# Kernel tuning notes

Measured on AMD Instinct MI355X. Metric: run time of the kernel, lower is better.

The kernel has to match this reference:

```python
import jax, jax.numpy as jnp
import numpy as np

ANCHORS = np.array([10,13,16,30,33,23,30,61,62,45,59,119,116,90,156,198,373,326], np.float32).reshape(-1, 2)
ANCHOR_MASK = ((6, 7, 8), (3, 4, 5), (0, 1, 2))
INPUT_SHAPE = (416.0, 416.0)
NUM_BOX = 3
NUM_CLASSES = 80
LOC_RATIO, CLS_RATIO, CONF_RATIO = 0.05, 0.5, 1.0
BALANCE = (0.4, 1.0, 4.0)
EPS = 1e-7


def _bce(p, t):
    p = jnp.clip(p, EPS, 1.0 - EPS)
    return -t * jnp.log(p) - (1.0 - t) * jnp.log(1.0 - p)


def _build_targets(i, targets_xywh, targets_cls, H, W):
    # Vectorized version of get_target: per-box anchor argmax-IoU matching
    # followed by scatter writes into the [B, 3, H, W, 5+C] target tensor.
    B, T, _ = targets_xywh.shape
    sy, sx = INPUT_SHAPE[0] / H, INPUT_SHAPE[1] / W
    sa = jnp.asarray(ANCHORS / np.array([sx, sy], np.float32))  # [9,2] scaled anchors
    bx = targets_xywh[..., 0] * W
    by = targets_xywh[..., 1] * H
    bw = targets_xywh[..., 2] * W
    bh = targets_xywh[..., 3] * H
    # IoU of zero-centered gt boxes vs zero-centered anchors reduces to min(w)*min(h)
    inter = jnp.minimum(bw[..., None], sa[:, 0]) * jnp.minimum(bh[..., None], sa[:, 1])
    union = (bw * bh)[..., None] + sa[:, 0] * sa[:, 1] - inter
    aid = jnp.argmax(inter / union, axis=-1)  # [B,T] best anchor of 9
    mrow = jnp.asarray(ANCHOR_MASK[i])  # i is a static Python int
    hit = aid[..., None] == mrow  # [B,T,3]
    valid = hit.any(-1)
    pos = jnp.argmax(hit, axis=-1)  # anchor_pos_id within this layer's mask
    gx = jnp.floor(bx).astype(jnp.int32)
    gy = jnp.floor(by).astype(jnp.int32)
    b_idx = jnp.broadcast_to(jnp.arange(B)[:, None], (B, T))
    b_sc = jnp.where(valid, b_idx, B)  # out-of-range batch index -> dropped scatter
    tw = jnp.log(bw / sa[aid, 0])
    th = jnp.log(bh / sa[aid, 1])
    y_true = jnp.zeros((B, NUM_BOX, H, W, 5 + NUM_CLASSES), jnp.float32)
    y_true = y_true.at[b_sc, pos, gy, gx, 0].set(bx - gx, mode='drop')
    y_true = y_true.at[b_sc, pos, gy, gx, 1].set(by - gy, mode='drop')
    y_true = y_true.at[b_sc, pos, gy, gx, 2].set(tw, mode='drop')
    y_true = y_true.at[b_sc, pos, gy, gx, 3].set(th, mode='drop')
    y_true = y_true.at[b_sc, pos, gy, gx, 5 + targets_cls].set(1.0, mode='drop')
    y_true = y_true.at[b_sc, pos, gy, gx, 4].set(1.0, mode='drop')
    loss_scale = jnp.zeros((B, NUM_BOX, H, W), jnp.float32)
    loss_scale = loss_scale.at[b_sc, pos, gy, gx].set(bw * bh / (H * W), mode='drop')
    return y_true, loss_scale


def setup_inputs() -> dict:
    key = jax.random.key(0)
    k1, k2, k3, k4 = jax.random.split(key, 4)
    B, T, H, W = 32, 50, 52, 52
    pred = jax.random.normal(k1, (B, NUM_BOX * (5 + NUM_CLASSES), H, W), jnp.float32) * 0.5
    xy = jax.random.uniform(k2, (B, T, 2), jnp.float32, 0.02, 0.98)
    wh = jax.random.uniform(k3, (B, T, 2), jnp.float32, 0.02, 0.5)
    targets_xywh = jnp.concatenate([xy, wh], axis=-1)
    targets_cls = jax.random.randint(k4, (B, T), 0, NUM_CLASSES, jnp.int32)
    return {"i": 2, "pred": pred, "targets_xywh": targets_xywh, "targets_cls": targets_cls}


def reference(i, pred, targets_xywh, targets_cls):
    B = pred.shape[0]
    H, W = pred.shape[-2:]
    y_true, loss_scale = _build_targets(i, targets_xywh, targets_cls, H, W)
    y_true = jax.lax.stop_gradient(y_true)  # torch builds these with requires_grad=False
    loss_scale = jax.lax.stop_gradient(loss_scale)
    # [B, 3*(5+C), H, W] -> [B, 3, H, W, 5+C]
    p = pred.reshape(B, NUM_BOX, 5 + NUM_CLASSES, H, W).transpose(0, 1, 3, 4, 2)
    x = jax.nn.sigmoid(p[..., 0])
    y = jax.nn.sigmoid(p[..., 1])
    w = p[..., 2]
    h = p[..., 3]
    conf = jax.nn.sigmoid(p[..., 4])
    cls_prob = jax.nn.sigmoid(p[..., 5:])
    scale = 2.0 - loss_scale
    m = (y_true[..., 4] == 1).astype(jnp.float32)
    pos_num = m.sum()
    den = jnp.maximum(pos_num, 1.0)
    lx = (_bce(x, y_true[..., 0]) * scale * m).sum() / den
    ly = (_bce(y, y_true[..., 1]) * scale * m).sum() / den
    lw = (jnp.square(w - y_true[..., 2]) * scale * m).sum() / den
    lh = (jnp.square(h - y_true[..., 3]) * scale * m).sum() / den
    loc_loss = (lx + ly + lh + lw) * 0.1
    cls_loss = (_bce(cls_prob, y_true[..., 5:]) * m[..., None]).sum() / (den * NUM_CLASSES)
    conf_loss = _bce(conf, y_true[..., 4]).mean() * BALANCE[i]
    has = pos_num > 0
    total = jnp.where(has, loc_loss * LOC_RATIO + cls_loss * CLS_RATIO, 0.0) + conf_loss * CONF_RATIO
    return jnp.stack([total, conf_loss, jnp.where(has, loc_loss, 0.0), jnp.where(has, cls_loss, 0.0)])
```

## Files before the change

### kernel.cpp

```cpp
#include <hip/hip_runtime.h>
#include <math.h>

#define BB 32
#define TT 50
#define HH 52
#define WW 52
#define NB 3
#define NC 80
#define CE 85
#define SP (HH*WW)
#define NCELL (BB*NB*SP)
#define NT (BB*TT)
#define EPSF 1e-7f

#define NBLK 507
#define POSBLK 100

__device__ __forceinline__ float sigc(float z) {
    float p = 1.0f / (1.0f + expf(-z));
    return fminf(fmaxf(p, EPSF), 1.0f - EPSF);
}

__device__ __forceinline__ float softplus(float z) {
    return fmaxf(z, 0.0f) + log1pf(expf(-fabsf(z)));
}

__device__ __forceinline__ unsigned getbit(unsigned m0, unsigned m1, unsigned m2, int c) {
    return (c < 32) ? ((m0 >> c) & 1u)
         : (c < 64) ? ((m1 >> (c - 32)) & 1u)
                    : ((m2 >> (c - 64)) & 1u);
}

__device__ __forceinline__ int match_target(const float* __restrict__ xywh,
                                            const int* __restrict__ cls,
                                            int i, int w,
                                            float* obx, float* oby,
                                            float* obw, float* obh, int* oaid) {
    const float A[18] = {10,13,16,30,33,23,30,61,62,45,59,119,116,90,156,198,373,326};
    float bx = xywh[w*4+0] * WW, by = xywh[w*4+1] * HH;
    float bw = xywh[w*4+2] * WW, bh = xywh[w*4+3] * HH;
    int aid = 0;
    float bi = -1.0f, bu = 1.0f;
    #pragma unroll
    for (int k = 0; k < 9; ++k) {
        float aw = A[2*k] * 0.125f, ah = A[2*k+1] * 0.125f;
        float inter = fminf(bw, aw) * fminf(bh, ah);
        float uni = bw * bh + aw * ah - inter;
        if (inter * bu > bi * uni) { bi = inter; bu = uni; aid = k; }
    }
    *obx = bx; *oby = by; *obw = bw; *obh = bh; *oaid = aid;
    int gx = (int)floorf(bx), gy = (int)floorf(by);
    if ((aid / 3) == (2 - i) && gx >= 0 && gx < WW && gy >= 0 && gy < HH) {
        int b = w / TT;
        int cell = ((b * NB + (aid % 3)) * HH + gy) * WW + gx;
        return (cell << 7) | cls[w];
    }
    return -1;
}

__global__ void __launch_bounds__(256)
k_main(const float* __restrict__ pred,
       const float* __restrict__ xywh,
       const int* __restrict__ cls,
       const int* __restrict__ pi,
       float* __restrict__ confpart,
       float* __restrict__ pospart) {
    __shared__ int epack[NT];
    __shared__ float sred[4];
    __shared__ float pred_red[4][8];
    int tid = threadIdx.x;
    int bid = blockIdx.x;
    int lane = tid & 63;
    int wid = tid >> 6;

    int base = (bid * 256 + tid) * 2;
    int ba = base / SP, sp = base % SP;
    float2 z2 = *(const float2*)(pred + ((size_t)ba * CE + 4) * SP + sp);
    float vconf = softplus(z2.x) + softplus(z2.y);

    if (bid < POSBLK) {
        int i = *pi;
        for (int w = tid; w < NT; w += 256) {
            float bx, by, bw, bh; int aid;
            epack[w] = match_target(xywh, cls, i, w, &bx, &by, &bw, &bh, &aid);
        }
        __syncthreads();

        float zprim[4], zsec[4];
        bool tval[4];
        #pragma unroll
        for (int t = 0; t < 4; ++t) {
            int wv = bid * 16 + wid * 4 + t;
            int ep = epack[wv];
            tval[t] = (ep >= 0);
            zprim[t] = 0.0f; zsec[t] = 0.0f;
            if (ep >= 0) {
                int cell = ep >> 7;
                int cba = cell / SP, csp = cell % SP;
                const float* pc = pred + (size_t)cba * CE * SP + csp;
                zprim[t] = pc[lane * SP];
                if (lane < CE - 64) zsec[t] = pc[(64 + lane) * SP];
            }
        }

        float acc[7] = {0.f, 0.f, 0.f, 0.f, 0.f, 0.f, 0.f};
        #pragma unroll
        for (int t = 0; t < 4; ++t) {
            if (!tval[t]) continue;
            int wv = bid * 16 + wid * 4 + t;
            int cell = epack[wv] >> 7;
            unsigned m0 = 0, m1 = 0, m2 = 0;
            int mx = -1;
            #pragma unroll
            for (int k = 0; k < NT / 64; ++k) {
                int e = lane + 64 * k;
                int ee = epack[e];
                if (ee >= 0 && (ee >> 7) == cell) {
                    int c = ee & 127;
                    if (c < 32) m0 |= 1u << c;
                    else if (c < 64) m1 |= 1u << (c - 32);
                    else m2 |= 1u << (c - 64);
                    mx = max(mx, e);
                }
            }
            #pragma unroll
            for (int off = 32; off; off >>= 1) {
                m0 |= __shfl_xor(m0, off);
                m1 |= __shfl_xor(m1, off);
                m2 |= __shfl_xor(m2, off);
                mx = max(mx, __shfl_xor(mx, off));
            }
            if (mx != wv) continue;

            const float A[18] = {10,13,16,30,33,23,30,61,62,45,59,119,116,90,156,198,373,326};
            float bx, by, bw, bh; int aid;
            (void)match_target(xywh, cls, i, wv, &bx, &by, &bw, &bh, &aid);
            float aw = A[2*aid] * 0.125f, ah = A[2*aid+1] * 0.125f;
            float gx = floorf(bx), gy = floorf(by);
            float tx = bx - gx, ty = by - gy;
            float tw = logf(bw / aw), th = logf(bh / ah);
            float scale = 2.0f - bw * bh / (float)(HH * WW);

            float z = zprim[t];
            float p = sigc(z);
            float prim;
            if (lane == 0)      prim = (-tx * logf(p) - (1.0f - tx) * logf(1.0f - p)) * scale;
            else if (lane == 1) prim = (-ty * logf(p) - (1.0f - ty) * logf(1.0f - p)) * scale;
            else if (lane == 2) { float d = z - tw; prim = d * d * scale; }
            else if (lane == 3) { float d = z - th; prim = d * d * scale; }
            else if (lane == 4) prim = -logf(p) + logf(1.0f - p);
            else {
                int c = lane - 5;
                prim = getbit(m0, m1, m2, c) ? -logf(p) : -logf(1.0f - p);
            }
            float sec = 0.0f;
            if (lane < CE - 64) {
                float pc2 = sigc(zsec[t]);
                sec = getbit(m0, m1, m2, 59 + lane) ? -logf(pc2) : -logf(1.0f - pc2);
            }
            float clsv = (lane >= 5 ? prim : 0.0f) + sec;
            #pragma unroll
            for (int off = 32; off; off >>= 1) clsv += __shfl_xor(clsv, off);
            acc[0] += __shfl(prim, 0);
            acc[1] += __shfl(prim, 1);
            acc[2] += __shfl(prim, 2);
            acc[3] += __shfl(prim, 3);
            acc[4] += __shfl(prim, 4);
            acc[5] += clsv;
            acc[6] += 1.0f;
        }
        if (lane == 0) {
            #pragma unroll
            for (int k = 0; k < 7; ++k) pred_red[wid][k] = acc[k];
        }
        __syncthreads();
        if (tid == 0) {
            float r[7];
            #pragma unroll
            for (int k = 0; k < 7; ++k)
                r[k] = pred_red[0][k] + pred_red[1][k] + pred_red[2][k] + pred_red[3][k];
            float4 a = make_float4(r[0], r[1], r[2], r[3]);
            float4 b = make_float4(r[4], r[5], r[6], 0.0f);
            *(float4*)(pospart + bid * 8)     = a;
            *(float4*)(pospart + bid * 8 + 4) = b;
        }
    }

    #pragma unroll
    for (int off = 32; off; off >>= 1) vconf += __shfl_down(vconf, off);
    if (lane == 0) sred[wid] = vconf;
    __syncthreads();
    if (tid == 0) confpart[bid] = sred[0] + sred[1] + sred[2] + sred[3];
}

__global__ void __launch_bounds__(256)
k_final(const float* __restrict__ confpart,
        const float* __restrict__ pospart,
        const int* __restrict__ pi,
        float* __restrict__ out) {
    int tid = threadIdx.x;
    float v[7] = {0.f, 0.f, 0.f, 0.f, 0.f, 0.f, 0.f};
    for (int r = tid; r < NBLK; r += 256) v[0] += confpart[r];
    if (tid < POSBLK) {
        float4 a = *(const float4*)(pospart + tid * 8);
        float4 b = *(const float4*)(pospart + tid * 8 + 4);
        v[1] += a.x; v[2] += a.y; v[3] += a.z; v[4] += a.w;
        v[0] += b.x; v[5] += b.y; v[6] += b.z;
    }
    #pragma unroll
    for (int off = 32; off; off >>= 1) {
        #pragma unroll
        for (int k = 0; k < 7; ++k) v[k] += __shfl_down(v[k], off);
    }
    __shared__ float red[4][7];
    int wid = tid >> 6, lane = tid & 63;
    if (lane == 0) {
        #pragma unroll
        for (int k = 0; k < 7; ++k) red[wid][k] = v[k];
    }
    __syncthreads();
    if (tid == 0) {
        float conf_s = red[0][0] + red[1][0] + red[2][0] + red[3][0];
        float lxs    = red[0][1] + red[1][1] + red[2][1] + red[3][1];
        float lys    = red[0][2] + red[1][2] + red[2][2] + red[3][2];
        float lws    = red[0][3] + red[1][3] + red[2][3] + red[3][3];
        float lhs    = red[0][4] + red[1][4] + red[2][4] + red[3][4];
        float cls_s  = red[0][5] + red[1][5] + red[2][5] + red[3][5];
        float pos    = red[0][6] + red[1][6] + red[2][6] + red[3][6];

        float den = fmaxf(pos, 1.0f);
        float loc = (lxs + lys + lws + lhs) / den * 0.1f;
        float clsL = cls_s / (den * (float)NC);
        int i = *pi;
        float bal = (i == 0) ? 0.4f : (i == 1) ? 1.0f : 4.0f;
        float conf = conf_s / (float)NCELL * bal;
        bool has = pos > 0.0f;
        float total = (has ? (loc * 0.05f + clsL * 0.5f) : 0.0f) + conf;
        out[0] = total;
        out[1] = conf;
        out[2] = has ? loc : 0.0f;
        out[3] = has ? clsL : 0.0f;
    }
}

extern "C" void kernel_launch(void* const* d_in, const int* in_sizes, int n_in,
                              void* d_out, int out_size, void* d_ws, size_t ws_size,
                              hipStream_t stream) {
    const int*   pi   = (const int*)d_in[0];
    const float* pred = (const float*)d_in[1];
    const float* xywh = (const float*)d_in[2];
    const int*   cls  = (const int*)d_in[3];
    float* out = (float*)d_out;

    char* ws = (char*)d_ws;
    float* confpart = (float*)ws;
    float* pospart  = (float*)(ws + 4096);

    k_main <<<NBLK, 256, 0, stream>>>(pred, xywh, cls, pi, confpart, pospart);
    k_final<<<1, 256, 0, stream>>>(confpart, pospart, pi, out);
}
```

Measured before the change: 19.49 us.

## Fuse final reduction into main kernel via last-block atomic counters

Removes the separate k_final launch. The last block to finish, detected through a two-level atomic counter tree (8 sub-counters, then a master counter), performs the final reduction inside k_main. Partial results are now published with atomicExch and read back with atomic adds of zero so they are coherent across blocks. This adds a hipMemsetAsync to reset the counters, plus atomic and serialization overhead in the tail block.

```diff
diff --git a/kernel.cpp b/kernel.cpp
--- a/kernel.cpp
+++ b/kernel.cpp
@@ -30,6 +30,8 @@
          : (c < 64) ? ((m1 >> (c - 32)) & 1u)
                     : ((m2 >> (c - 64)) & 1u);
 }
+
+__device__ __forceinline__ float crd(float* p) { return atomicAdd(p, 0.0f); }
 
 __device__ __forceinline__ int match_target(const float* __restrict__ xywh,
                                             const int* __restrict__ cls,
@@ -63,11 +65,16 @@
        const float* __restrict__ xywh,
        const int* __restrict__ cls,
        const int* __restrict__ pi,
+       unsigned* __restrict__ cnt_sub,
+       unsigned* __restrict__ cnt_mst,
        float* __restrict__ confpart,
-       float* __restrict__ pospart) {
+       float* __restrict__ pospart,
+       float* __restrict__ out) {
     __shared__ int epack[NT];
     __shared__ float sred[4];
     __shared__ float pred_red[4][8];
+    __shared__ float fred[4][7];
+    __shared__ unsigned slast;
     int tid = threadIdx.x;
     int bid = blockIdx.x;
     int lane = tid & 63;
@@ -175,14 +182,13 @@
         }
         __syncthreads();
         if (tid == 0) {
-            float r[7];
-            #pragma unroll
-            for (int k = 0; k < 7; ++k)
-                r[k] = pred_red[0][k] + pred_red[1][k] + pred_red[2][k] + pred_red[3][k];
-            float4 a = make_float4(r[0], r[1], r[2], r[3]);
-            float4 b = make_float4(r[4], r[5], r[6], 0.0f);
-            *(float4*)(pospart + bid * 8)     = a;
-            *(float4*)(pospart + bid * 8 + 4) = b;
+            float sink = 0.0f;
+            #pragma unroll
+            for (int k = 0; k < 7; ++k) {
+                float r = pred_red[0][k] + pred_red[1][k] + pred_red[2][k] + pred_red[3][k];
+                sink += atomicExch(&pospart[bid * 8 + k], r);
+            }
+            asm volatile("" :: "v"(sink));
         }
     }
 
@@ -190,56 +196,69 @@
     for (int off = 32; off; off >>= 1) vconf += __shfl_down(vconf, off);
     if (lane == 0) sred[wid] = vconf;
     __syncthreads();
-    if (tid == 0) confpart[bid] = sred[0] + sred[1] + sred[2] + sred[3];
-}
-
-__global__ void __launch_bounds__(256)
-k_final(const float* __restrict__ confpart,
-        const float* __restrict__ pospart,
-        const int* __restrict__ pi,
-        float* __restrict__ out) {
-    int tid = threadIdx.x;
-    float v[7] = {0.f, 0.f, 0.f, 0.f, 0.f, 0.f, 0.f};
-    for (int r = tid; r < NBLK; r += 256) v[0] += confpart[r];
-    if (tid < POSBLK) {
-        float4 a = *(const float4*)(pospart + tid * 8);
-        float4 b = *(const float4*)(pospart + tid * 8 + 4);
-        v[1] += a.x; v[2] += a.y; v[3] += a.z; v[4] += a.w;
-        v[0] += b.x; v[5] += b.y; v[6] += b.z;
-    }
-    #pragma unroll
-    for (int off = 32; off; off >>= 1) {
+
+    if (tid == 0) {
+        float cp = sred[0] + sred[1] + sred[2] + sred[3];
+        float old = atomicExch(&confpart[bid], cp);
+        asm volatile("" :: "v"(old));
+        asm volatile("s_waitcnt vmcnt(0)" ::: "memory");
+        int j = bid & 7;
+        unsigned quota = (j < 3) ? 64u : 63u;
+        unsigned o = atomicAdd(&cnt_sub[j], 1u);
+        unsigned last = 0u;
+        if (o == quota - 1u) {
+            asm volatile("s_waitcnt vmcnt(0)" ::: "memory");
+            unsigned om = atomicAdd(cnt_mst, 1u);
+            last = (om == 7u) ? 1u : 0u;
+        }
+        slast = last;
+    }
+    __syncthreads();
+
+    if (slast) {
+        float v[7] = {0.f, 0.f, 0.f, 0.f, 0.f, 0.f, 0.f};
+        for (int r = tid; r < NBLK; r += 256) v[0] += crd(&confpart[r]);
+        if (tid < POSBLK) {
+            v[1] += crd(&pospart[tid * 8 + 0]);
+            v[2] += crd(&pospart[tid * 8 + 1]);
+            v[3] += crd(&pospart[tid * 8 + 2]);
+            v[4] += crd(&pospart[tid * 8 + 3]);
+            v[0] += crd(&pospart[tid * 8 + 4]);
+            v[5] += crd(&pospart[tid * 8 + 5]);
+            v[6] += crd(&pospart[tid * 8 + 6]);
+        }
         #pragma unroll
-        for (int k = 0; k < 7; ++k) v[k] += __shfl_down(v[k], off);
-    }
-    __shared__ float red[4][7];
-    int wid = tid >> 6, lane = tid & 63;
-    if (lane == 0) {
-        #pragma unroll
-        for (int k = 0; k < 7; ++k) red[wid][k] = v[k];
-    }
-    __syncthreads();
-    if (tid == 0) {
-        float conf_s = red[0][0] + red[1][0] + red[2][0] + red[3][0];
-        float lxs    = red[0][1] + red[1][1] + red[2][1] + red[3][1];
-        float lys    = red[0][2] + red[1][2] + red[2][2] + red[3][2];
-        float lws    = red[0][3] + red[1][3] + red[2][3] + red[3][3];
-        float lhs    = red[0][4] + red[1][4] + red[2][4] + red[3][4];
-        float cls_s  = red[0][5] + red[1][5] + red[2][5] + red[3][5];
-        float pos    = red[0][6] + red[1][6] + red[2][6] + red[3][6];
-
-        float den = fmaxf(pos, 1.0f);
-        float loc = (lxs + lys + lws + lhs) / den * 0.1f;
-        float clsL = cls_s / (den * (float)NC);
-        int i = *pi;
-        float bal = (i == 0) ? 0.4f : (i == 1) ? 1.0f : 4.0f;
-        float conf = conf_s / (float)NCELL * bal;
-        bool has = pos > 0.0f;
-        float total = (has ? (loc * 0.05f + clsL * 0.5f) : 0.0f) + conf;
-        out[0] = total;
-        out[1] = conf;
-        out[2] = has ? loc : 0.0f;
-        out[3] = has ? clsL : 0.0f;
+        for (int off = 32; off; off >>= 1) {
+            #pragma unroll
+            for (int k = 0; k < 7; ++k) v[k] += __shfl_down(v[k], off);
+        }
+        if (lane == 0) {
+            #pragma unroll
+            for (int k = 0; k < 7; ++k) fred[wid][k] = v[k];
+        }
+        __syncthreads();
+        if (tid == 0) {
+            float conf_s = fred[0][0] + fred[1][0] + fred[2][0] + fred[3][0];
+            float lxs    = fred[0][1] + fred[1][1] + fred[2][1] + fred[3][1];
+            float lys    = fred[0][2] + fred[1][2] + fred[2][2] + fred[3][2];
+            float lws    = fred[0][3] + fred[1][3] + fred[2][3] + fred[3][3];
+            float lhs    = fred[0][4] + fred[1][4] + fred[2][4] + fred[3][4];
+            float cls_s  = fred[0][5] + fred[1][5] + fred[2][5] + fred[3][5];
+            float pos    = fred[0][6] + fred[1][6] + fred[2][6] + fred[3][6];
+
+            float den = fmaxf(pos, 1.0f);
+            float loc = (lxs + lys + lws + lhs) / den * 0.1f;
+            float clsL = cls_s / (den * (float)NC);
+            int i = *pi;
+            float bal = (i == 0) ? 0.4f : (i == 1) ? 1.0f : 4.0f;
+            float conf = conf_s / (float)NCELL * bal;
+            bool has = pos > 0.0f;
+            float total = (has ? (loc * 0.05f + clsL * 0.5f) : 0.0f) + conf;
+            out[0] = total;
+            out[1] = conf;
+            out[2] = has ? loc : 0.0f;
+            out[3] = has ? clsL : 0.0f;
+        }
     }
 }
 
@@ -253,9 +272,12 @@
     float* out = (float*)d_out;
 
     char* ws = (char*)d_ws;
-    float* confpart = (float*)ws;
-    float* pospart  = (float*)(ws + 4096);
-
-    k_main <<<NBLK, 256, 0, stream>>>(pred, xywh, cls, pi, confpart, pospart);
-    k_final<<<1, 256, 0, stream>>>(confpart, pospart, pi, out);
-}
+    unsigned* cnt_sub  = (unsigned*)ws;
+    unsigned* cnt_mst  = (unsigned*)(ws + 32);
+    float*    confpart = (float*)(ws + 256);
+    float*    pospart  = (float*)(ws + 4096);
+
+    hipMemsetAsync(ws, 0, 64, stream);
+    k_main<<<NBLK, 256, 0, stream>>>(pred, xywh, cls, pi,
+                                     cnt_sub, cnt_mst, confpart, pospart, out);
+}
```

Result: slower. 29.23 us (+50.0%).
